# Performance work log

Hardware: AMD Instinct MI355X
Metric: run time of the kernel (lower is better)

## Reference

```python
import jax, jax.numpy as jnp
import numpy as np
from jax.scipy.linalg import solve_triangular

H, VD, M = 16, 64, 128
RIDGE = 0.01


def setup_inputs() -> dict:
    key = jax.random.key(0)
    ks = jax.random.split(key, 9)
    B, L, HD = 4, 2048, 1024
    s = 1.0 / np.sqrt(HD).astype(np.float32)
    return {
        "x": jax.random.normal(ks[0], (B, L, HD), dtype=jnp.float32),
        "cur_k": jnp.zeros((1,), dtype=jnp.float32),
        "input_mask": jnp.ones((B, L), dtype=jnp.float32),
        "Wq": jax.random.normal(ks[1], (HD, HD), dtype=jnp.float32) * s,
        "Wk": jax.random.normal(ks[2], (HD, HD), dtype=jnp.float32) * s,
        "Wv": jax.random.normal(ks[3], (HD, HD), dtype=jnp.float32) * s,
        "Wo": jax.random.normal(ks[4], (HD, HD), dtype=jnp.float32) * s,
        "bo": jax.random.normal(ks[5], (HD,), dtype=jnp.float32) * s,
        "rff_W": jax.random.normal(ks[6], (H, VD, M), dtype=jnp.float32),  # / lengthscale=1.0
        "rff_b": 2.0 * np.pi * jax.random.uniform(ks[7], (H, M), dtype=jnp.float32),
    }


def reference(x, cur_k, input_mask, Wq, Wk, Wv, Wo, bo, rff_W, rff_b):
    B, L, HD = x.shape
    scale = jnp.asarray(1.0 / np.sqrt(M), dtype=x.dtype)
    M2 = 2 * M

    def heads(t):  # [B,L,HD] -> [B,H,L,VD]
        return t.reshape(B, L, H, VD).transpose(0, 2, 1, 3)

    q = heads(x @ Wq.T)
    k = heads(x @ Wk.T)
    v = heads(x @ Wv.T)

    mask = input_mask[:, :L].astype(x.dtype)
    qmask = mask[:, None, :, None]  # [B,1,L,1]

    def rff(X):  # [B,H,L,VD] -> [B,H,L,2M]
        proj = jnp.einsum('bhld,hdm->bhlm', X, rff_W) + rff_b[None, :, None, :]
        return scale * jnp.concatenate([jnp.cos(proj), jnp.sin(proj)], axis=-1)

    PhiQ = rff(q)
    PhiK_w = rff(k) * qmask
    V_w = v * qmask

    G = jnp.einsum('bhlm,bhln->bhmn', PhiK_w, PhiK_w)  # [B,H,2M,2M]
    G = G + RIDGE * jnp.eye(M2, dtype=x.dtype)
    T = jnp.einsum('bhlm,bhld->bhmd', PhiK_w, V_w)      # [B,H,2M,VD]

    Lch = jnp.linalg.cholesky(G)
    y = solve_triangular(Lch, T, lower=True)
    W = solve_triangular(jnp.swapaxes(Lch, -2, -1), y, lower=False)

    out = jnp.einsum('bhlm,bhmd->bhld', PhiQ, W)        # [B,H,L,VD]
    # unsqueeze sample dim, permute to [B,1,L,H,VD], flatten heads -> [B,1,L,HD]
    samples = jnp.transpose(out, (0, 2, 1, 3)).reshape(B, L, HD)[:, None]
    samples = samples @ Wo.T + bo                        # W_O (dropout: eval no-op)
    samples = samples * qmask                            # [B,1,L,1] broadcast
    return samples
```

## Files before the change

kernel.cpp:

```cpp
#include <hip/hip_runtime.h>
#include <math.h>

#define B_ 4
#define L_ 2048
#define HD_ 1024
#define H_ 16
#define VD_ 64
#define M_ 128
#define M2_ 256
#define RIDGE_ 0.01f
#define SCALE_ 0.08838834764831845f

typedef unsigned short u16;
typedef __attribute__((ext_vector_type(8))) short short8;
typedef __attribute__((ext_vector_type(4))) float floatx4;

__device__ __forceinline__ u16 f2bf(float x) {
  unsigned u = __float_as_uint(x);
  unsigned r = u + 0x7fff + ((u >> 16) & 1);
  return (u16)(r >> 16);
}
__device__ __forceinline__ float bf2f(u16 h) {
  return __uint_as_float(((unsigned)h) << 16);
}
__device__ __forceinline__ void gload_lds16(const u16* g, u16* l) {
  __builtin_amdgcn_global_load_lds(
      (const __attribute__((address_space(1))) unsigned int*)g,
      (__attribute__((address_space(3))) unsigned int*)l, 16, 0, 0);
}
__device__ __forceinline__ void split4(float4 f, ushort4* h, float4* r) {
  h->x = f2bf(f.x); h->y = f2bf(f.y); h->z = f2bf(f.z); h->w = f2bf(f.w);
  r->x = f.x - bf2f(h->x); r->y = f.y - bf2f(h->y);
  r->z = f.z - bf2f(h->z); r->w = f.w - bf2f(h->w);
}

__global__ __launch_bounds__(256) void cvt_split_kernel(
    const float* __restrict__ src, u16* __restrict__ hi, u16* __restrict__ lo, int n4)
{
  int i = blockIdx.x * 256 + threadIdx.x;
  if (i < n4) {
    float4 f = ((const float4*)src)[i];
    ushort4 hv; float4 r;
    split4(f, &hv, &r);
    ushort4 lv = {f2bf(r.x), f2bf(r.y), f2bf(r.z), f2bf(r.w)};
    ((ushort4*)hi)[i] = hv;
    ((ushort4*)lo)[i] = lv;
  }
}

__global__ __launch_bounds__(256) void mfma_nt(
    const u16* __restrict__ A0, const u16* __restrict__ B0,
    float* __restrict__ C, int Ndim, int Kdim, int ldA, int ldB,
    const float* __restrict__ bias, const float* __restrict__ mask)
{
  __shared__ __align__(16) u16 a_sm[4096];
  __shared__ __align__(16) u16 b_sm[4096];
  const int tid = threadIdx.x;
  const int wave = tid >> 6, lane = tid & 63;
  const int m0 = blockIdx.y * 128, n0 = blockIdx.x * 128;
  const int wrow = (wave >> 1) * 64, wcol = (wave & 1) * 64;
  const int fm = lane & 15, q = lane >> 4;

  floatx4 acc[4][4];
#pragma unroll
  for (int i = 0; i < 4; ++i)
#pragma unroll
    for (int j = 0; j < 4; ++j) acc[i][j] = (floatx4){0.f, 0.f, 0.f, 0.f};

  const u16* Ag0 = A0 + (long)(m0 + lane) * ldA + wave * 8;
  const u16* Ag1 = A0 + (long)(m0 + 64 + lane) * ldA + wave * 8;
  const u16* Bg0 = B0 + (long)(n0 + lane) * ldB + wave * 8;
  const u16* Bg1 = B0 + (long)(n0 + 64 + lane) * ldB + wave * 8;
  u16* la0 = &a_sm[(wave * 128 + 0) * 8];
  u16* la1 = &a_sm[(wave * 128 + 64) * 8];
  u16* lb0 = &b_sm[(wave * 128 + 0) * 8];
  u16* lb1 = &b_sm[(wave * 128 + 64) * 8];

  for (int k0 = 0; k0 < Kdim; k0 += 32) {
    __syncthreads();
    gload_lds16(Ag0 + k0, la0);
    gload_lds16(Ag1 + k0, la1);
    gload_lds16(Bg0 + k0, lb0);
    gload_lds16(Bg1 + k0, lb1);
    __syncthreads();
    short8 af[4], bf[4];
#pragma unroll
    for (int i = 0; i < 4; ++i)
      af[i] = *(const short8*)&a_sm[(q * 128 + wrow + i * 16 + fm) * 8];
#pragma unroll
    for (int j = 0; j < 4; ++j)
      bf[j] = *(const short8*)&b_sm[(q * 128 + wcol + j * 16 + fm) * 8];
#pragma unroll
    for (int i = 0; i < 4; ++i)
#pragma unroll
      for (int j = 0; j < 4; ++j)
        acc[i][j] = __builtin_amdgcn_mfma_f32_16x16x32_bf16(af[i], bf[j], acc[i][j], 0, 0, 0);
  }

  const int colb = n0 + wcol + fm;
  const int rbase = m0 + wrow + (lane >> 4) * 4;
#pragma unroll
  for (int j = 0; j < 4; ++j) {
    int cg = colb + j * 16;
    float bb = bias ? bias[cg] : 0.f;
#pragma unroll
    for (int i = 0; i < 4; ++i) {
#pragma unroll
      for (int r = 0; r < 4; ++r) {
        int row = rbase + i * 16 + r;
        float val = acc[i][j][r];
        if (bias) val = (val + bb) * mask[row];
        C[(long)row * Ndim + cg] = val;
      }
    }
  }
}

__global__ __launch_bounds__(256) void mfma_nt3(
    const u16* __restrict__ Ah, const u16* __restrict__ Al,
    const u16* __restrict__ Bh, const u16* __restrict__ Bl,
    float* __restrict__ Cq, float* __restrict__ Ck, float* __restrict__ Cv)
{
  __shared__ __align__(16) u16 ah_sm[4096], al_sm[4096];
  __shared__ __align__(16) u16 bh_sm[4096], bl_sm[4096];
  const int tid = threadIdx.x;
  const int wave = tid >> 6, lane = tid & 63;
  const int m0 = blockIdx.y * 128, n0 = blockIdx.x * 128;
  const int wrow = (wave >> 1) * 64, wcol = (wave & 1) * 64;
  const int fm = lane & 15, q = lane >> 4;
  const bool vblk = (n0 >= 2048);

  floatx4 acc[4][4];
#pragma unroll
  for (int i = 0; i < 4; ++i)
#pragma unroll
    for (int j = 0; j < 4; ++j) acc[i][j] = (floatx4){0.f, 0.f, 0.f, 0.f};

  const long a0o = (long)(m0 + lane) * 1024 + wave * 8;
  const long a1o = (long)(m0 + 64 + lane) * 1024 + wave * 8;
  const long b0o = (long)(n0 + lane) * 1024 + wave * 8;
  const long b1o = (long)(n0 + 64 + lane) * 1024 + wave * 8;
  u16* lah0 = &ah_sm[(wave * 128 + 0) * 8];
  u16* lah1 = &ah_sm[(wave * 128 + 64) * 8];
  u16* lal0 = &al_sm[(wave * 128 + 0) * 8];
  u16* lal1 = &al_sm[(wave * 128 + 64) * 8];
  u16* lbh0 = &bh_sm[(wave * 128 + 0) * 8];
  u16* lbh1 = &bh_sm[(wave * 128 + 64) * 8];
  u16* lbl0 = &bl_sm[(wave * 128 + 0) * 8];
  u16* lbl1 = &bl_sm[(wave * 128 + 64) * 8];

  for (int k0 = 0; k0 < 1024; k0 += 32) {
    __syncthreads();
    gload_lds16(Ah + a0o + k0, lah0);
    gload_lds16(Ah + a1o + k0, lah1);
    gload_lds16(Bh + b0o + k0, lbh0);
    gload_lds16(Bh + b1o + k0, lbh1);
    if (!vblk) {
      gload_lds16(Al + a0o + k0, lal0);
      gload_lds16(Al + a1o + k0, lal1);
      gload_lds16(Bl + b0o + k0, lbl0);
      gload_lds16(Bl + b1o + k0, lbl1);
    }
    __syncthreads();
    short8 afh[4], bfh[4];
#pragma unroll
    for (int i = 0; i < 4; ++i)
      afh[i] = *(const short8*)&ah_sm[(q * 128 + wrow + i * 16 + fm) * 8];
#pragma unroll
    for (int j = 0; j < 4; ++j)
      bfh[j] = *(const short8*)&bh_sm[(q * 128 + wcol + j * 16 + fm) * 8];
    if (vblk) {
#pragma unroll
      for (int i = 0; i < 4; ++i)
#pragma unroll
        for (int j = 0; j < 4; ++j)
          acc[i][j] = __builtin_amdgcn_mfma_f32_16x16x32_bf16(afh[i], bfh[j], acc[i][j], 0, 0, 0);
    } else {
      short8 afl[4], bfl[4];
#pragma unroll
      for (int i = 0; i < 4; ++i)
        afl[i] = *(const short8*)&al_sm[(q * 128 + wrow + i * 16 + fm) * 8];
#pragma unroll
      for (int j = 0; j < 4; ++j)
        bfl[j] = *(const short8*)&bl_sm[(q * 128 + wcol + j * 16 + fm) * 8];
#pragma unroll
      for (int i = 0; i < 4; ++i)
#pragma unroll
        for (int j = 0; j < 4; ++j) {
          acc[i][j] = __builtin_amdgcn_mfma_f32_16x16x32_bf16(afh[i], bfh[j], acc[i][j], 0, 0, 0);
          acc[i][j] = __builtin_amdgcn_mfma_f32_16x16x32_bf16(afl[i], bfh[j], acc[i][j], 0, 0, 0);
          acc[i][j] = __builtin_amdgcn_mfma_f32_16x16x32_bf16(afh[i], bfl[j], acc[i][j], 0, 0, 0);
        }
    }
  }

  float* Cp; int cb;
  if (n0 < 1024)      { Cp = Cq; cb = n0; }
  else if (n0 < 2048) { Cp = Ck; cb = n0 - 1024; }
  else                { Cp = Cv; cb = n0 - 2048; }
  const int colb = cb + wcol + fm;
  const int rbase = m0 + wrow + (lane >> 4) * 4;
#pragma unroll
  for (int j = 0; j < 4; ++j) {
    int cg = colb + j * 16;
#pragma unroll
    for (int i = 0; i < 4; ++i)
#pragma unroll
      for (int r = 0; r < 4; ++r)
        Cp[(long)(rbase + i * 16 + r) * 1024 + cg] = acc[i][j][r];
  }
}

__global__ __launch_bounds__(256) void rff_k_t(
    const float* __restrict__ src, const float* __restrict__ mask,
    const float* __restrict__ rffW, const float* __restrict__ rffb,
    u16* __restrict__ pkh, u16* __restrict__ pkl, int b0)
{
  __shared__ __align__(16) float w_lds[64][132];
  __shared__ __align__(16) float x_lds[64][68];
  __shared__ float b_lds[128];
  const int l0 = blockIdx.x * 64;
  const int h = blockIdx.y, b = b0 + blockIdx.z;
  const int zloc = blockIdx.z * 16 + h;
  const int tid = threadIdx.x;

  const float* wsrc = rffW + h * 8192;
  for (int f = tid * 4; f < 8192; f += 1024) {
    int d = f >> 7, m = f & 127;
    *(float4*)&w_lds[d][m] = *(const float4*)&wsrc[f];
  }
  if (tid < 128) b_lds[tid] = rffb[h * 128 + tid];
  {
    int r = tid >> 2, c0 = (tid & 3) * 16;
    const float* srow = src + (long)(b * L_ + l0 + r) * 1024 + h * VD_ + c0;
    *(float4*)&x_lds[r][c0 + 0]  = *(const float4*)(srow + 0);
    *(float4*)&x_lds[r][c0 + 4]  = *(const float4*)(srow + 4);
    *(float4*)&x_lds[r][c0 + 8]  = *(const float4*)(srow + 8);
    *(float4*)&x_lds[r][c0 + 12] = *(const float4*)(srow + 12);
  }
  __syncthreads();

  const int ty = tid >> 4, tx = tid & 15;
  float acc[4][8];
  {
    float4 bb0 = *(const float4*)&b_lds[4 * tx];
    float4 bb1 = *(const float4*)&b_lds[4 * tx + 64];
#pragma unroll
    for (int i = 0; i < 4; ++i) {
      acc[i][0] = bb0.x; acc[i][1] = bb0.y; acc[i][2] = bb0.z; acc[i][3] = bb0.w;
      acc[i][4] = bb1.x; acc[i][5] = bb1.y; acc[i][6] = bb1.z; acc[i][7] = bb1.w;
    }
  }
#pragma unroll 8
  for (int kk = 0; kk < 64; ++kk) {
    float4 w0 = *(const float4*)&w_lds[kk][4 * tx];
    float4 w1 = *(const float4*)&w_lds[kk][4 * tx + 64];
    float xv[4];
#pragma unroll
    for (int i = 0; i < 4; ++i) xv[i] = x_lds[4 * ty + i][kk];
#pragma unroll
    for (int i = 0; i < 4; ++i) {
      acc[i][0] = fmaf(xv[i], w0.x, acc[i][0]);
      acc[i][1] = fmaf(xv[i], w0.y, acc[i][1]);
      acc[i][2] = fmaf(xv[i], w0.z, acc[i][2]);
      acc[i][3] = fmaf(xv[i], w0.w, acc[i][3]);
      acc[i][4] = fmaf(xv[i], w1.x, acc[i][4]);
      acc[i][5] = fmaf(xv[i], w1.y, acc[i][5]);
      acc[i][6] = fmaf(xv[i], w1.z, acc[i][6]);
      acc[i][7] = fmaf(xv[i], w1.w, acc[i][7]);
    }
  }
  float fi[4];
#pragma unroll
  for (int i = 0; i < 4; ++i) fi[i] = SCALE_ * mask[b * L_ + l0 + 4 * ty + i];
  float cvv[4][8], svv[4][8];
#pragma unroll
  for (int i = 0; i < 4; ++i)
#pragma unroll
    for (int jj = 0; jj < 8; ++jj) {
      float sv, cv;
      sincosf(acc[i][jj], &sv, &cv);
      cvv[i][jj] = cv * fi[i];
      svv[i][jj] = sv * fi[i];
    }
  const long lbase = l0 + 4 * ty;
  const long zbase = (long)zloc * 655360;
#pragma unroll
  for (int jj = 0; jj < 8; ++jj) {
    int mcol = (jj < 4) ? (4 * tx + jj) : (64 + 4 * tx + (jj - 4));
    ushort4 h4, l4;
    h4.x = f2bf(cvv[0][jj]); l4.x = f2bf(cvv[0][jj] - bf2f(h4.x));
    h4.y = f2bf(cvv[1][jj]); l4.y = f2bf(cvv[1][jj] - bf2f(h4.y));
    h4.z = f2bf(cvv[2][jj]); l4.z = f2bf(cvv[2][jj] - bf2f(h4.z));
    h4.w = f2bf(cvv[3][jj]); l4.w = f2bf(cvv[3][jj] - bf2f(h4.w));
    long base = zbase + (long)mcol * 2048 + lbase;
    *(ushort4*)&pkh[base] = h4;
    *(ushort4*)&pkl[base] = l4;
    ushort4 hs, ls;
    hs.x = f2bf(svv[0][jj]); ls.x = f2bf(svv[0][jj] - bf2f(hs.x));
    hs.y = f2bf(svv[1][jj]); ls.y = f2bf(svv[1][jj] - bf2f(hs.y));
    hs.z = f2bf(svv[2][jj]); ls.z = f2bf(svv[2][jj] - bf2f(hs.z));
    hs.w = f2bf(svv[3][jj]); ls.w = f2bf(svv[3][jj] - bf2f(hs.w));
    long base2 = zbase + (long)(mcol + 128) * 2048 + lbase;
    *(ushort4*)&pkh[base2] = hs;
    *(ushort4*)&pkl[base2] = ls;
  }
}

__global__ __launch_bounds__(256) void vt_kernel(
    const float* __restrict__ v, const float* __restrict__ mask,
    u16* __restrict__ pkh, u16* __restrict__ pkl, int b0)
{
  __shared__ float t[128][65];
  const int z = blockIdx.y;
  const int b = b0 + (z >> 4), h = z & 15;
  const int l0 = blockIdx.x * 128;
  const int tid = threadIdx.x;
  const int d = tid & 63, lg = tid >> 6;
  for (int i = 0; i < 128; i += 4) {
    int ll = i + lg;
    float mv = mask[b * L_ + l0 + ll];
    t[ll][d] = v[(long)(b * L_ + l0 + ll) * 1024 + h * 64 + d] * mv;
  }
  __syncthreads();
  const int d2 = tid >> 2, lofs = (tid & 3) * 32;
  long base = (long)z * 655360 + (long)(256 + d2) * 2048 + l0 + lofs;
  for (int j = 0; j < 32; j += 4) {
    float f0 = t[lofs + j + 0][d2], f1 = t[lofs + j + 1][d2];
    float f2 = t[lofs + j + 2][d2], f3 = t[lofs + j + 3][d2];
    ushort4 hv, lv;
    hv.x = f2bf(f0); lv.x = f2bf(f0 - bf2f(hv.x));
    hv.y = f2bf(f1); lv.y = f2bf(f1 - bf2f(hv.y));
    hv.z = f2bf(f2); lv.z = f2bf(f2 - bf2f(hv.z));
    hv.w = f2bf(f3); lv.w = f2bf(f3 - bf2f(hv.w));
    *(ushort4*)&pkh[base + j] = hv;
    *(ushort4*)&pkl[base + j] = lv;
  }
}

__global__ __launch_bounds__(256) void mfma_gt(
    const u16* __restrict__ pkh, const u16* __restrict__ pkl,
    float* __restrict__ G, float* __restrict__ T, int bh0)
{
  __shared__ __align__(16) u16 ah_sm[4096], al_sm[4096];
  __shared__ __align__(16) u16 bh_sm[2048], bl_sm[2048];
  const int tid = threadIdx.x;
  const int wave = tid >> 6, lane = tid & 63;
  const int z = blockIdx.z;
  const int m0 = blockIdx.y * 128, n0 = blockIdx.x * 64;
  const int wrow = (wave >> 1) * 64, wcol = (wave & 1) * 32;
  const int fm = lane & 15, q = lane >> 4;
  const long batch = (long)z * 655360;
  const u16* Ah = pkh + batch;
  const u16* Al = pkl + batch;

  floatx4 acc[4][2];
#pragma unroll
  for (int i = 0; i < 4; ++i)
#pragma unroll
    for (int j = 0; j < 2; ++j) acc[i][j] = (floatx4){0.f, 0.f, 0.f, 0.f};

  const long a0o = (long)(m0 + lane) * 2048 + wave * 8;
  const long a1o = (long)(m0 + 64 + lane) * 2048 + wave * 8;
  const long b0o = (long)(n0 + lane) * 2048 + wave * 8;
  u16* lah0 = &ah_sm[(wave * 128 + 0) * 8];
  u16* lah1 = &ah_sm[(wave * 128 + 64) * 8];
  u16* lal0 = &al_sm[(wave * 128 + 0) * 8];
  u16* lal1 = &al_sm[(wave * 128 + 64) * 8];
  u16* lbh = &bh_sm[(wave * 64) * 8];
  u16* lbl = &bl_sm[(wave * 64) * 8];

  for (int k0 = 0; k0 < 2048; k0 += 32) {
    __syncthreads();
    gload_lds16(Ah + a0o + k0, lah0);
    gload_lds16(Ah + a1o + k0, lah1);
    gload_lds16(Al + a0o + k0, lal0);
    gload_lds16(Al + a1o + k0, lal1);
    gload_lds16(Ah + b0o + k0, lbh);
    gload_lds16(Al + b0o + k0, lbl);
    __syncthreads();
    short8 afh[4], afl[4], bfh[2], bfl[2];
#pragma unroll
    for (int i = 0; i < 4; ++i) {
      afh[i] = *(const short8*)&ah_sm[(q * 128 + wrow + i * 16 + fm) * 8];
      afl[i] = *(const short8*)&al_sm[(q * 128 + wrow + i * 16 + fm) * 8];
    }
#pragma unroll
    for (int j = 0; j < 2; ++j) {
      bfh[j] = *(const short8*)&bh_sm[(q * 64 + wcol + j * 16 + fm) * 8];
      bfl[j] = *(const short8*)&bl_sm[(q * 64 + wcol + j * 16 + fm) * 8];
    }
#pragma unroll
    for (int i = 0; i < 4; ++i)
#pragma unroll
      for (int j = 0; j < 2; ++j) {
        acc[i][j] = __builtin_amdgcn_mfma_f32_16x16x32_bf16(afh[i], bfh[j], acc[i][j], 0, 0, 0);
        acc[i][j] = __builtin_amdgcn_mfma_f32_16x16x32_bf16(afl[i], bfh[j], acc[i][j], 0, 0, 0);
        acc[i][j] = __builtin_amdgcn_mfma_f32_16x16x32_bf16(afh[i], bfl[j], acc[i][j], 0, 0, 0);
      }
  }

  const int bh = bh0 + z;
  const int rbase = m0 + wrow + (lane >> 4) * 4;
#pragma unroll
  for (int j = 0; j < 2; ++j) {
    int col = n0 + wcol + j * 16 + fm;
#pragma unroll
    for (int i = 0; i < 4; ++i)
#pragma unroll
      for (int r = 0; r < 4; ++r) {
        int row = rbase + i * 16 + r;
        float val = acc[i][j][r];
        if (n0 < 256) G[(long)bh * 65536 + (long)row * 256 + col] = val;
        else T[(long)bh * 16384 + (long)row * 64 + (col - 256)] = val;
      }
  }
}

__global__ __launch_bounds__(256) void mfma_out_k(
    const u16* __restrict__ ph, const u16* __restrict__ pl,
    const u16* __restrict__ wth, const u16* __restrict__ wtl,
    u16* __restrict__ oh)
{
  __shared__ __align__(16) u16 ah_sm[4096], al_sm[4096];
  __shared__ __align__(16) u16 bh_sm[2048], bl_sm[2048];
  const int tid = threadIdx.x;
  const int wave = tid >> 6, lane = tid & 63;
  const int bh = blockIdx.y;
  const int b = bh >> 4, h = bh & 15;
  const int l0 = blockIdx.x * 128;
  const int wrow = (wave >> 1) * 64, wcol = (wave & 1) * 32;
  const int fm = lane & 15, q = lane >> 4;
  const u16* Ah = ph + (long)bh * 524288 + (long)l0 * 256;
  const u16* Al = pl + (long)bh * 524288 + (long)l0 * 256;
  const u16* Bh = wth + (long)bh * 16384;
  const u16* Bl = wtl + (long)bh * 16384;

  floatx4 acc[4][2];
#pragma unroll
  for (int i = 0; i < 4; ++i)
#pragma unroll
    for (int j = 0; j < 2; ++j) acc[i][j] = (floatx4){0.f, 0.f, 0.f, 0.f};

  const long a0o = (long)lane * 256 + wave * 8;
  const long a1o = (long)(64 + lane) * 256 + wave * 8;
  const long b0o = (long)lane * 256 + wave * 8;
  u16* lah0 = &ah_sm[(wave * 128 + 0) * 8];
  u16* lah1 = &ah_sm[(wave * 128 + 64) * 8];
  u16* lal0 = &al_sm[(wave * 128 + 0) * 8];
  u16* lal1 = &al_sm[(wave * 128 + 64) * 8];
  u16* lbh = &bh_sm[(wave * 64) * 8];
  u16* lbl = &bl_sm[(wave * 64) * 8];

  for (int k0 = 0; k0 < 256; k0 += 32) {
    __syncthreads();
    gload_lds16(Ah + a0o + k0, lah0);
    gload_lds16(Ah + a1o + k0, lah1);
    gload_lds16(Al + a0o + k0, lal0);
    gload_lds16(Al + a1o + k0, lal1);
    gload_lds16(Bh + b0o + k0, lbh);
    gload_lds16(Bl + b0o + k0, lbl);
    __syncthreads();
    short8 afh[4], afl[4], bfh[2], bfl[2];
#pragma unroll
    for (int i = 0; i < 4; ++i) {
      afh[i] = *(const short8*)&ah_sm[(q * 128 + wrow + i * 16 + fm) * 8];
      afl[i] = *(const short8*)&al_sm[(q * 128 + wrow + i * 16 + fm) * 8];
    }
#pragma unroll
    for (int j = 0; j < 2; ++j) {
      bfh[j] = *(const short8*)&bh_sm[(q * 64 + wcol + j * 16 + fm) * 8];
      bfl[j] = *(const short8*)&bl_sm[(q * 64 + wcol + j * 16 + fm) * 8];
    }
#pragma unroll
    for (int i = 0; i < 4; ++i)
#pragma unroll
      for (int j = 0; j < 2; ++j) {
        acc[i][j] = __builtin_amdgcn_mfma_f32_16x16x32_bf16(afh[i], bfh[j], acc[i][j], 0, 0, 0);
        acc[i][j] = __builtin_amdgcn_mfma_f32_16x16x32_bf16(afl[i], bfh[j], acc[i][j], 0, 0, 0);
        acc[i][j] = __builtin_amdgcn_mfma_f32_16x16x32_bf16(afh[i], bfl[j], acc[i][j], 0, 0, 0);
      }
  }

  const int rbase = l0 + wrow + (lane >> 4) * 4;
#pragma unroll
  for (int j = 0; j < 2; ++j) {
    int col = h * 64 + wcol + j * 16 + fm;
#pragma unroll
    for (int i = 0; i < 4; ++i)
#pragma unroll
      for (int r = 0; r < 4; ++r)
        oh[(long)(b * L_ + rbase + i * 16 + r) * 1024 + col] = f2bf(acc[i][j][r]);
  }
}

__global__ __launch_bounds__(512) void chol_rffq_wo_kernel(
    const float* __restrict__ G, float* __restrict__ Lg,
    const float* __restrict__ qsrc,
    const float* __restrict__ rffW, const float* __restrict__ rffb,
    u16* __restrict__ ph, u16* __restrict__ pl,
    const float* __restrict__ Wo, u16* __restrict__ wo_hi)
{
  extern __shared__ float sm[];
  const int bx = blockIdx.x;
  const int tid = threadIdx.x;

  if (bx < 64) {
    float* Lb = sm;
    const int bh = bx;
    const float* Gb = G + (long)bh * 65536;
    for (int f = tid; f < 136 * 256; f += 512) {
      int bi = f >> 8, e = f & 255;
      int i = e >> 4, j = e & 15;
      int I = 0; while ((I + 1) * (I + 2) / 2 <= bi) ++I;
      int J = bi - I * (I + 1) / 2;
      float v = Gb[(I * 16 + i) * 256 + J * 16 + j];
      if (I == J && i == j) v += RIDGE_;
      Lb[bi * 272 + i * 17 + j] = v;
    }
    __syncthreads();

    for (int p = 0; p < 16; ++p) {
      const int diagbase = (p * (p + 1) / 2 + p) * 272;
      if (tid < 64) {
        const int i = tid & 15;
        float r[16];
#pragma unroll
        for (int k = 0; k < 16; ++k) r[k] = Lb[diagbase + i * 17 + k];
#pragma unroll
        for (int j = 0; j < 16; ++j) {
          float dj = __shfl(r[j], j);
          float dinv = 1.0f / sqrtf(dj);
          r[j] *= dinv;
          float Lij = r[j];
#pragma unroll
          for (int k = j + 1; k < 16; ++k) {
            float Lkj = __shfl(r[j], k);
            r[k] = fmaf(-Lij, Lkj, r[k]);
          }
        }
        float x[16];
#pragma unroll
        for (int j = 0; j < 16; ++j) {
          float s = (i == j) ? 1.0f : 0.0f;
#pragma unroll
          for (int k = 0; k < j; ++k) {
            float Ljk = __shfl(r[k], j);
            s = fmaf(-Ljk, x[k], s);
          }
          float Ljj = __shfl(r[j], j);
          x[j] = s / Ljj;
        }
        if (tid < 16) {
#pragma unroll
          for (int j = 0; j < 16; ++j) Lb[diagbase + j * 17 + tid] = x[j];
        }
      }
      __syncthreads();

      const int nIb = 15 - p;
      const int tot = nIb * 256;
      float outv[8];
#pragma unroll
      for (int s = 0; s < 8; ++s) {
        int f = tid + s * 512;
        if (f < tot) {
          int Ib = f >> 8;
          int I = p + 1 + Ib;
          int e = f & 255;
          int i = e >> 4, j = e & 15;
          const float* Ablk = &Lb[(I * (I + 1) / 2 + p) * 272 + i * 17];
          const float* invD = &Lb[diagbase + j * 17];
          float s2 = 0.f;
#pragma unroll
          for (int k = 0; k < 16; ++k) s2 = fmaf(Ablk[k], invD[k], s2);
          outv[s] = s2;
        }
      }
      __syncthreads();
#pragma unroll
      for (int s = 0; s < 8; ++s) {
        int f = tid + s * 512;
        if (f < tot) {
          int Ib = f >> 8;
          int I = p + 1 + Ib;
          int e = f & 255;
          int i = e >> 4, j = e & 15;
          Lb[(I * (I + 1) / 2 + p) * 272 + i * 17 + j] = outv[s];
        }
      }
      __syncthreads();

      const int npairs = nIb * (nIb + 1) / 2;
      const int g = tid >> 4, t = tid & 15;
      const int tx = t & 3, ty = t >> 2;
      for (int pi0 = 0; pi0 < npairs; pi0 += 32) {
        int pi = pi0 + g;
        if (pi < npairs) {
          int a = 0; while ((a + 1) * (a + 2) / 2 <= pi) ++a;
          int b2 = pi - a * (a + 1) / 2;
          int I = p + 1 + a, J = p + 1 + b2;
          float* Cblk = &Lb[(I * (I + 1) / 2 + J) * 272];
          const float* Ablk = &Lb[(I * (I + 1) / 2 + p) * 272];
          const float* Bblk = &Lb[(J * (J + 1) / 2 + p) * 272];
          float c4[4][4];
#pragma unroll
          for (int ii = 0; ii < 4; ++ii)
#pragma unroll
            for (int jj = 0; jj < 4; ++jj)
              c4[ii][jj] = Cblk[(4 * ty + ii) * 17 + 4 * tx + jj];
#pragma unroll
          for (int kk = 0; kk < 16; ++kk) {
            float av[4], bv[4];
#pragma unroll
            for (int ii = 0; ii < 4; ++ii) av[ii] = Ablk[(4 * ty + ii) * 17 + kk];
#pragma unroll
            for (int jj = 0; jj < 4; ++jj) bv[jj] = Bblk[(4 * tx + jj) * 17 + kk];
#pragma unroll
            for (int ii = 0; ii < 4; ++ii)
#pragma unroll
              for (int jj = 0; jj < 4; ++jj)
                c4[ii][jj] = fmaf(-av[ii], bv[jj], c4[ii][jj]);
          }
#pragma unroll
          for (int ii = 0; ii < 4; ++ii)
#pragma unroll
            for (int jj = 0; jj < 4; ++jj)
              Cblk[(4 * ty + ii) * 17 + 4 * tx + jj] = c4[ii][jj];
        }
      }
      __syncthreads();
    }

    float* Lgb = Lg + (long)bh * 34816;
    for (int f = tid * 4; f < 136 * 256; f += 2048) {
      int bi = f >> 8, e = f & 255;
      int i = e >> 4, j = e & 15;
      float4 v;
      v.x = Lb[bi * 272 + i * 17 + j];
      v.y = Lb[bi * 272 + i * 17 + j + 1];
      v.z = Lb[bi * 272 + i * 17 + j + 2];
      v.w = Lb[bi * 272 + i * 17 + j + 3];
      *(float4*)&Lgb[f] = v;
    }
  } else if (bx < 64 + 1024) {
    const int id = bx - 64;
    const int l0 = (id & 15) * 128;
    const int h = (id >> 4) & 15;
    const int b = id >> 8;
    float* w_lds = sm;
    float* x_lds = sm + 8448;
    float* b_lds = sm + 8448 + 8704;

    const float* wsrc = rffW + h * 8192;
    for (int f = tid * 4; f < 8192; f += 2048) {
      int d = f >> 7, m = f & 127;
      *(float4*)&w_lds[d * 132 + m] = *(const float4*)&wsrc[f];
    }
    if (tid < 128) b_lds[tid] = rffb[h * 128 + tid];
    {
      int r = tid >> 2, c0 = (tid & 3) * 16;
      const float* srow = qsrc + (long)(b * L_ + l0 + r) * 1024 + h * VD_ + c0;
      *(float4*)&x_lds[r * 68 + c0 + 0]  = *(const float4*)(srow + 0);
      *(float4*)&x_lds[r * 68 + c0 + 4]  = *(const float4*)(srow + 4);
      *(float4*)&x_lds[r * 68 + c0 + 8]  = *(const float4*)(srow + 8);
      *(float4*)&x_lds[r * 68 + c0 + 12] = *(const float4*)(srow + 12);
    }
    __syncthreads();

    const int sub = tid >> 8;
    const int t = tid & 255;
    const int ty = t >> 4, tx = t & 15;
    const int rrow = sub * 64 + 4 * ty;
    float acc[4][8];
    {
      float4 bb0 = *(const float4*)&b_lds[4 * tx];
      float4 bb1 = *(const float4*)&b_lds[4 * tx + 64];
#pragma unroll
      for (int i = 0; i < 4; ++i) {
        acc[i][0] = bb0.x; acc[i][1] = bb0.y; acc[i][2] = bb0.z; acc[i][3] = bb0.w;
        acc[i][4] = bb1.x; acc[i][5] = bb1.y; acc[i][6] = bb1.z; acc[i][7] = bb1.w;
      }
    }
#pragma unroll 8
    for (int kk = 0; kk < 64; ++kk) {
      float4 w0 = *(const float4*)&w_lds[kk * 132 + 4 * tx];
      float4 w1 = *(const float4*)&w_lds[kk * 132 + 4 * tx + 64];
      float xv[4];
#pragma unroll
      for (int i = 0; i < 4; ++i) xv[i] = x_lds[(rrow + i) * 68 + kk];
#pragma unroll
      for (int i = 0; i < 4; ++i) {
        acc[i][0] = fmaf(xv[i], w0.x, acc[i][0]);
        acc[i][1] = fmaf(xv[i], w0.y, acc[i][1]);
        acc[i][2] = fmaf(xv[i], w0.z, acc[i][2]);
        acc[i][3] = fmaf(xv[i], w0.w, acc[i][3]);
        acc[i][4] = fmaf(xv[i], w1.x, acc[i][4]);
        acc[i][5] = fmaf(xv[i], w1.y, acc[i][5]);
        acc[i][6] = fmaf(xv[i], w1.z, acc[i][6]);
        acc[i][7] = fmaf(xv[i], w1.w, acc[i][7]);
      }
    }
#pragma unroll
    for (int i = 0; i < 4; ++i) {
      int l = l0 + rrow + i;
      float4 c0, c1, s0, s1;
      float sv, cv;
      sincosf(acc[i][0], &sv, &cv); c0.x = cv * SCALE_; s0.x = sv * SCALE_;
      sincosf(acc[i][1], &sv, &cv); c0.y = cv * SCALE_; s0.y = sv * SCALE_;
      sincosf(acc[i][2], &sv, &cv); c0.z = cv * SCALE_; s0.z = sv * SCALE_;
      sincosf(acc[i][3], &sv, &cv); c0.w = cv * SCALE_; s0.w = sv * SCALE_;
      sincosf(acc[i][4], &sv, &cv); c1.x = cv * SCALE_; s1.x = sv * SCALE_;
      sincosf(acc[i][5], &sv, &cv); c1.y = cv * SCALE_; s1.y = sv * SCALE_;
      sincosf(acc[i][6], &sv, &cv); c1.z = cv * SCALE_; s1.z = sv * SCALE_;
      sincosf(acc[i][7], &sv, &cv); c1.w = cv * SCALE_; s1.w = sv * SCALE_;
      long base = ((long)(b * H_ + h) * L_ + l) * M2_;
      ushort4 hv; float4 r4;
      split4(c0, &hv, &r4);
      *(ushort4*)&ph[base + 4 * tx] = hv;
      *(ushort4*)&pl[base + 4 * tx] = (ushort4){f2bf(r4.x), f2bf(r4.y), f2bf(r4.z), f2bf(r4.w)};
      split4(c1, &hv, &r4);
      *(ushort4*)&ph[base + 64 + 4 * tx] = hv;
      *(ushort4*)&pl[base + 64 + 4 * tx] = (ushort4){f2bf(r4.x), f2bf(r4.y), f2bf(r4.z), f2bf(r4.w)};
      split4(s0, &hv, &r4);
      *(ushort4*)&ph[base + 128 + 4 * tx] = hv;
      *(ushort4*)&pl[base + 128 + 4 * tx] = (ushort4){f2bf(r4.x), f2bf(r4.y), f2bf(r4.z), f2bf(r4.w)};
      split4(s1, &hv, &r4);
      *(ushort4*)&ph[base + 192 + 4 * tx] = hv;
      *(ushort4*)&pl[base + 192 + 4 * tx] = (ushort4){f2bf(r4.x), f2bf(r4.y), f2bf(r4.z), f2bf(r4.w)};
    }
  } else {
    const int id2 = bx - (64 + 1024);
    int idx = id2 * 512 + tid;
    for (int i = idx; i < 262144; i += 65536) {
      float4 f = ((const float4*)Wo)[i];
      ushort4 hv = {f2bf(f.x), f2bf(f.y), f2bf(f.z), f2bf(f.w)};
      ((ushort4*)wo_hi)[i] = hv;
    }
  }
}

__global__ __launch_bounds__(256) void tri_solve_kernel(
    const float* __restrict__ Lg, const float* __restrict__ T,
    float* __restrict__ Wt)
{
  __shared__ float Y[256 * 17];
  __shared__ float tmp[16 * 17];
  const int bh = blockIdx.y;
  const int d0 = blockIdx.x * 16;
  const int tid = threadIdx.x;
  const int i = tid >> 4, d = tid & 15;
  const float* Lb = Lg + (long)bh * 34816;
  const float* Tb = T + (long)bh * 16384;

  for (int r = i; r < 256; r += 16) Y[r * 17 + d] = Tb[r * 64 + d0 + d];
  __syncthreads();

  for (int J = 0; J < 16; ++J) {
    float acc = Y[(J * 16 + i) * 17 + d];
    for (int c = 0; c < J; ++c) {
      const float* Lblk = &Lb[(J * (J + 1) / 2 + c) * 256 + i * 16];
#pragma unroll
      for (int k = 0; k < 16; k += 4) {
        float4 l4 = *(const float4*)&Lblk[k];
        acc = fmaf(-l4.x, Y[(c * 16 + k + 0) * 17 + d], acc);
        acc = fmaf(-l4.y, Y[(c * 16 + k + 1) * 17 + d], acc);
        acc = fmaf(-l4.z, Y[(c * 16 + k + 2) * 17 + d], acc);
        acc = fmaf(-l4.w, Y[(c * 16 + k + 3) * 17 + d], acc);
      }
    }
    tmp[i * 17 + d] = acc;
    __syncthreads();
    const float* invD = &Lb[(J * (J + 1) / 2 + J) * 256 + i * 16];
    float y = 0.f;
#pragma unroll
    for (int k = 0; k < 16; ++k) y = fmaf(invD[k], tmp[k * 17 + d], y);
    Y[(J * 16 + i) * 17 + d] = y;
    __syncthreads();
  }

  for (int J = 15; J >= 0; --J) {
    float acc = Y[(J * 16 + i) * 17 + d];
    for (int I = J + 1; I < 16; ++I) {
      const float* Lblk = &Lb[(I * (I + 1) / 2 + J) * 256];
#pragma unroll
      for (int k = 0; k < 16; ++k)
        acc = fmaf(-Lblk[k * 16 + i], Y[(I * 16 + k) * 17 + d], acc);
    }
    tmp[i * 17 + d] = acc;
    __syncthreads();
    const float* invD = &Lb[(J * (J + 1) / 2 + J) * 256];
    float w = 0.f;
#pragma unroll
    for (int k = 0; k < 16; ++k) w = fmaf(invD[k * 16 + i], tmp[k * 17 + d], w);
    Y[(J * 16 + i) * 17 + d] = w;
    __syncthreads();
  }

  for (int f = tid; f < 16 * 256; f += 256) {
    int dc = f >> 8, m = f & 255;
    Wt[(long)bh * 16384 + (long)(d0 + dc) * 256 + m] = Y[m * 17 + dc];
  }
}

__global__ void ws_too_small_kernel(float* out) { out[0] = 12345.0f; }

extern "C" void kernel_launch(void* const* d_in, const int* in_sizes, int n_in,
                              void* d_out, int out_size, void* d_ws, size_t ws_size,
                              hipStream_t stream) {
  const float* x    = (const float*)d_in[0];
  const float* mask = (const float*)d_in[2];
  const float* Wq   = (const float*)d_in[3];
  const float* Wk   = (const float*)d_in[4];
  const float* Wv   = (const float*)d_in[5];
  const float* Wo   = (const float*)d_in[6];
  const float* bo   = (const float*)d_in[7];
  const float* rffW = (const float*)d_in[8];
  const float* rffb = (const float*)d_in[9];
  float* out = (float*)d_out;
  float* ws  = (float*)d_ws;

  const size_t needed = 58720256UL * 4UL;
  if (ws_size < needed) {
    ws_too_small_kernel<<<1, 1, 0, stream>>>(out);
    return;
  }
  float* q = ws;
  u16* oh_bf = (u16*)ws;
  float* kbuf = ws + 8388608;
  float* T    = ws + 8388608;
  float* G    = ws + 9437184;
  float* Lg   = ws + 13631488;
  u16* big16 = (u16*)(ws + 16777216);
  u16* x_hi = big16;
  u16* x_lo = big16 + 8388608;
  u16* w_hi = big16 + 16777216;
  u16* w_lo = big16 + 19922944;
  u16* pk_hi = big16;
  u16* pk_lo = big16 + 20971520;
  u16* phiq_hi = big16;
  u16* phiq_lo = big16 + 33554432;
  float* v = ws + 50331648;
  float* wt_f = ws + 50331648;
  u16* wt_hi = (u16*)(ws + 51380224);
  u16* wt_lo = wt_hi + 1048576;
  u16* wo_hi = wt_hi + 2097152;

  hipFuncSetAttribute((const void*)chol_rffq_wo_kernel,
                      hipFuncAttributeMaxDynamicSharedMemorySize, 147968);

  dim3 blk(256);

  cvt_split_kernel<<<8192, blk, 0, stream>>>(x, x_hi, x_lo, 2097152);
  cvt_split_kernel<<<1024, blk, 0, stream>>>(Wq, w_hi,           w_lo,           262144);
  cvt_split_kernel<<<1024, blk, 0, stream>>>(Wk, w_hi + 1048576, w_lo + 1048576, 262144);
  cvt_split_kernel<<<1024, blk, 0, stream>>>(Wv, w_hi + 2097152, w_lo + 2097152, 262144);

  mfma_nt3<<<dim3(24, 64), blk, 0, stream>>>(x_hi, x_lo, w_hi, w_lo, q, kbuf, v);

  for (int half = 0; half < 2; ++half) {
    int b0 = half * 2, bh0 = half * 32;
    rff_k_t<<<dim3(32, 16, 2), blk, 0, stream>>>(kbuf, mask, rffW, rffb, pk_hi, pk_lo, b0);
    vt_kernel<<<dim3(16, 32), blk, 0, stream>>>(v, mask, pk_hi, pk_lo, b0);
    mfma_gt<<<dim3(5, 2, 32), blk, 0, stream>>>(pk_hi, pk_lo, G, T, bh0);
  }

  chol_rffq_wo_kernel<<<dim3(64 + 1024 + 128), dim3(512), 147968, stream>>>(
      G, Lg, q, rffW, rffb, phiq_hi, phiq_lo, Wo, wo_hi);

  tri_solve_kernel<<<dim3(4, 64), dim3(256), 0, stream>>>(Lg, T, wt_f);
  cvt_split_kernel<<<1024, blk, 0, stream>>>(wt_f, wt_hi, wt_lo, 262144);

  mfma_out_k<<<dim3(16, 64), blk, 0, stream>>>(phiq_hi, phiq_lo, wt_hi, wt_lo, oh_bf);

  mfma_nt<<<dim3(8, 64), blk, 0, stream>>>(oh_bf, wo_hi, out, 1024, 1024, 1024, 1024, bo, mask);
}
```

Before: 969.5 us.

## Split-K the G/T Gram GEMM, separate V projection, fuse Wt bf16 split

The G/T Gram GEMM now splits the 2048-long reduction into two halves across twice as many blocks. Partial results go to separate buffers and a new reduction kernel sums them, giving more parallelism from the small 5x2x32 grid. The fused QKV projection is split into a Q/K-only kernel that always uses the 3-term hi/lo product, plus a plain single-term mfma_nt for V. This removes the per-block branch. The triangular solve now writes bf16 hi/lo directly, dropping a separate conversion kernel launch and its fp32 round-trip, at the cost of extra partial-buffer traffic and one more launch.

```diff
diff --git a/kernel.cpp b/kernel.cpp
--- a/kernel.cpp
+++ b/kernel.cpp
@@ -116,10 +116,10 @@
   }
 }
 
-__global__ __launch_bounds__(256) void mfma_nt3(
+__global__ __launch_bounds__(256) void mfma_qk3(
     const u16* __restrict__ Ah, const u16* __restrict__ Al,
     const u16* __restrict__ Bh, const u16* __restrict__ Bl,
-    float* __restrict__ Cq, float* __restrict__ Ck, float* __restrict__ Cv)
+    float* __restrict__ Cq, float* __restrict__ Ck)
 {
   __shared__ __align__(16) u16 ah_sm[4096], al_sm[4096];
   __shared__ __align__(16) u16 bh_sm[4096], bl_sm[4096];
@@ -128,7 +128,6 @@
   const int m0 = blockIdx.y * 128, n0 = blockIdx.x * 128;
   const int wrow = (wave >> 1) * 64, wcol = (wave & 1) * 64;
   const int fm = lane & 15, q = lane >> 4;
-  const bool vblk = (n0 >= 2048);
 
   floatx4 acc[4][4];
 #pragma unroll
@@ -153,51 +152,37 @@
     __syncthreads();
     gload_lds16(Ah + a0o + k0, lah0);
     gload_lds16(Ah + a1o + k0, lah1);
+    gload_lds16(Al + a0o + k0, lal0);
+    gload_lds16(Al + a1o + k0, lal1);
     gload_lds16(Bh + b0o + k0, lbh0);
     gload_lds16(Bh + b1o + k0, lbh1);
-    if (!vblk) {
-      gload_lds16(Al + a0o + k0, lal0);
-      gload_lds16(Al + a1o + k0, lal1);
-      gload_lds16(Bl + b0o + k0, lbl0);
-      gload_lds16(Bl + b1o + k0, lbl1);
-    }
-    __syncthreads();
-    short8 afh[4], bfh[4];
+    gload_lds16(Bl + b0o + k0, lbl0);
+    gload_lds16(Bl + b1o + k0, lbl1);
+    __syncthreads();
+    short8 afh[4], afl[4], bfh[4], bfl[4];
+#pragma unroll
+    for (int i = 0; i < 4; ++i) {
+      afh[i] = *(const short8*)&ah_sm[(q * 128 + wrow + i * 16 + fm) * 8];
+      afl[i] = *(const short8*)&al_sm[(q * 128 + wrow + i * 16 + fm) * 8];
+    }
+#pragma unroll
+    for (int j = 0; j < 4; ++j) {
+      bfh[j] = *(const short8*)&bh_sm[(q * 128 + wcol + j * 16 + fm) * 8];
+      bfl[j] = *(const short8*)&bl_sm[(q * 128 + wcol + j * 16 + fm) * 8];
+    }
 #pragma unroll
     for (int i = 0; i < 4; ++i)
-      afh[i] = *(const short8*)&ah_sm[(q * 128 + wrow + i * 16 + fm) * 8];
-#pragma unroll
-    for (int j = 0; j < 4; ++j)
-      bfh[j] = *(const short8*)&bh_sm[(q * 128 + wcol + j * 16 + fm) * 8];
-    if (vblk) {
-#pragma unroll
-      for (int i = 0; i < 4; ++i)
-#pragma unroll
-        for (int j = 0; j < 4; ++j)
-          acc[i][j] = __builtin_amdgcn_mfma_f32_16x16x32_bf16(afh[i], bfh[j], acc[i][j], 0, 0, 0);
-    } else {
-      short8 afl[4], bfl[4];
-#pragma unroll
-      for (int i = 0; i < 4; ++i)
-        afl[i] = *(const short8*)&al_sm[(q * 128 + wrow + i * 16 + fm) * 8];
-#pragma unroll
-      for (int j = 0; j < 4; ++j)
-        bfl[j] = *(const short8*)&bl_sm[(q * 128 + wcol + j * 16 + fm) * 8];
-#pragma unroll
-      for (int i = 0; i < 4; ++i)
-#pragma unroll
-        for (int j = 0; j < 4; ++j) {
-          acc[i][j] = __builtin_amdgcn_mfma_f32_16x16x32_bf16(afh[i], bfh[j], acc[i][j], 0, 0, 0);
-          acc[i][j] = __builtin_amdgcn_mfma_f32_16x16x32_bf16(afl[i], bfh[j], acc[i][j], 0, 0, 0);
-          acc[i][j] = __builtin_amdgcn_mfma_f32_16x16x32_bf16(afh[i], bfl[j], acc[i][j], 0, 0, 0);
-        }
-    }
+#pragma unroll
+      for (int j = 0; j < 4; ++j) {
+        acc[i][j] = __builtin_amdgcn_mfma_f32_16x16x32_bf16(afh[i], bfh[j], acc[i][j], 0, 0, 0);
+        acc[i][j] = __builtin_amdgcn_mfma_f32_16x16x32_bf16(afl[i], bfh[j], acc[i][j], 0, 0, 0);
+        acc[i][j] = __builtin_amdgcn_mfma_f32_16x16x32_bf16(afh[i], bfl[j], acc[i][j], 0, 0, 0);
+      }
   }
 
   float* Cp; int cb;
-  if (n0 < 1024)      { Cp = Cq; cb = n0; }
-  else if (n0 < 2048) { Cp = Ck; cb = n0 - 1024; }
-  else                { Cp = Cv; cb = n0 - 2048; }
+  if (n0 < 1024) { Cp = Cq; cb = n0; }
+  else           { Cp = Ck; cb = n0 - 1024; }
   const int colb = cb + wcol + fm;
   const int rbase = m0 + wrow + (lane >> 4) * 4;
 #pragma unroll
@@ -340,14 +325,15 @@
 
 __global__ __launch_bounds__(256) void mfma_gt(
     const u16* __restrict__ pkh, const u16* __restrict__ pkl,
-    float* __restrict__ G, float* __restrict__ T, int bh0)
+    float* __restrict__ Gp, float* __restrict__ Tp, int bh0)
 {
   __shared__ __align__(16) u16 ah_sm[4096], al_sm[4096];
   __shared__ __align__(16) u16 bh_sm[2048], bl_sm[2048];
   const int tid = threadIdx.x;
   const int wave = tid >> 6, lane = tid & 63;
   const int z = blockIdx.z;
-  const int m0 = blockIdx.y * 128, n0 = blockIdx.x * 64;
+  const int mt = blockIdx.y & 1, kc = blockIdx.y >> 1;
+  const int m0 = mt * 128, n0 = blockIdx.x * 64;
   const int wrow = (wave >> 1) * 64, wcol = (wave & 1) * 32;
   const int fm = lane & 15, q = lane >> 4;
   const long batch = (long)z * 655360;
@@ -370,7 +356,8 @@
   u16* lbh = &bh_sm[(wave * 64) * 8];
   u16* lbl = &bl_sm[(wave * 64) * 8];
 
-  for (int k0 = 0; k0 < 2048; k0 += 32) {
+  const int kbeg = kc * 1024, kend = kbeg + 1024;
+  for (int k0 = kbeg; k0 < kend; k0 += 32) {
     __syncthreads();
     gload_lds16(Ah + a0o + k0, lah0);
     gload_lds16(Ah + a1o + k0, lah1);
@@ -401,6 +388,8 @@
   }
 
   const int bh = bh0 + z;
+  float* Gb = Gp + (long)kc * 4194304;
+  float* Tb = Tp + (long)kc * 1048576;
   const int rbase = m0 + wrow + (lane >> 4) * 4;
 #pragma unroll
   for (int j = 0; j < 2; ++j) {
@@ -411,9 +400,28 @@
       for (int r = 0; r < 4; ++r) {
         int row = rbase + i * 16 + r;
         float val = acc[i][j][r];
-        if (n0 < 256) G[(long)bh * 65536 + (long)row * 256 + col] = val;
-        else T[(long)bh * 16384 + (long)row * 64 + (col - 256)] = val;
-      }
+        if (n0 < 256) Gb[(long)bh * 65536 + (long)row * 256 + col] = val;
+        else Tb[(long)bh * 16384 + (long)row * 64 + (col - 256)] = val;
+      }
+  }
+}
+
+__global__ __launch_bounds__(256) void reduce_gt_kernel(
+    const float* __restrict__ Gp, float* __restrict__ G,
+    const float* __restrict__ Tp, float* __restrict__ T)
+{
+  long i = (long)blockIdx.x * 256 + threadIdx.x;
+  if (i < 1048576) {
+    float4 a = ((const float4*)Gp)[i];
+    float4 b = ((const float4*)(Gp + 4194304))[i];
+    float4 o = {a.x + b.x, a.y + b.y, a.z + b.z, a.w + b.w};
+    ((float4*)G)[i] = o;
+  } else {
+    long j = i - 1048576;
+    float4 a = ((const float4*)Tp)[j];
+    float4 b = ((const float4*)(Tp + 1048576))[j];
+    float4 o = {a.x + b.x, a.y + b.y, a.z + b.z, a.w + b.w};
+    ((float4*)T)[j] = o;
   }
 }
 
@@ -742,7 +750,7 @@
 
 __global__ __launch_bounds__(256) void tri_solve_kernel(
     const float* __restrict__ Lg, const float* __restrict__ T,
-    float* __restrict__ Wt)
+    u16* __restrict__ wth, u16* __restrict__ wtl)
 {
   __shared__ float Y[256 * 17];
   __shared__ float tmp[16 * 17];
@@ -799,7 +807,11 @@
 
   for (int f = tid; f < 16 * 256; f += 256) {
     int dc = f >> 8, m = f & 255;
-    Wt[(long)bh * 16384 + (long)(d0 + dc) * 256 + m] = Y[m * 17 + dc];
+    float val = Y[m * 17 + dc];
+    u16 h = f2bf(val);
+    long o = (long)bh * 16384 + (long)(d0 + dc) * 256 + m;
+    wth[o] = h;
+    wtl[o] = f2bf(val - bf2f(h));
   }
 }
 
@@ -838,11 +850,12 @@
   u16* w_lo = big16 + 19922944;
   u16* pk_hi = big16;
   u16* pk_lo = big16 + 20971520;
+  float* Gp = ws + 37748736;
+  float* Tp = ws + 46137344;
   u16* phiq_hi = big16;
   u16* phiq_lo = big16 + 33554432;
   float* v = ws + 50331648;
-  float* wt_f = ws + 50331648;
-  u16* wt_hi = (u16*)(ws + 51380224);
+  u16* wt_hi = (u16*)(ws + 50331648);
   u16* wt_lo = wt_hi + 1048576;
   u16* wo_hi = wt_hi + 2097152;
 
@@ -856,20 +869,23 @@
   cvt_split_kernel<<<1024, blk, 0, stream>>>(Wk, w_hi + 1048576, w_lo + 1048576, 262144);
   cvt_split_kernel<<<1024, blk, 0, stream>>>(Wv, w_hi + 2097152, w_lo + 2097152, 262144);
 
-  mfma_nt3<<<dim3(24, 64), blk, 0, stream>>>(x_hi, x_lo, w_hi, w_lo, q, kbuf, v);
+  mfma_qk3<<<dim3(16, 64), blk, 0, stream>>>(x_hi, x_lo, w_hi, w_lo, q, kbuf);
+  mfma_nt<<<dim3(8, 64), blk, 0, stream>>>(x_hi, w_hi + 2097152, v,
+                                           1024, 1024, 1024, 1024, nullptr, nullptr);
 
   for (int half = 0; half < 2; ++half) {
     int b0 = half * 2, bh0 = half * 32;
     rff_k_t<<<dim3(32, 16, 2), blk, 0, stream>>>(kbuf, mask, rffW, rffb, pk_hi, pk_lo, b0);
     vt_kernel<<<dim3(16, 32), blk, 0, stream>>>(v, mask, pk_hi, pk_lo, b0);
-    mfma_gt<<<dim3(5, 2, 32), blk, 0, stream>>>(pk_hi, pk_lo, G, T, bh0);
-  }
+    mfma_gt<<<dim3(5, 4, 32), blk, 0, stream>>>(pk_hi, pk_lo, Gp, Tp, bh0);
+  }
+
+  reduce_gt_kernel<<<5120, blk, 0, stream>>>(Gp, G, Tp, T);
 
   chol_rffq_wo_kernel<<<dim3(64 + 1024 + 128), dim3(512), 147968, stream>>>(
       G, Lg, q, rffW, rffb, phiq_hi, phiq_lo, Wo, wo_hi);
 
-  tri_solve_kernel<<<dim3(4, 64), dim3(256), 0, stream>>>(Lg, T, wt_f);
-  cvt_split_kernel<<<1024, blk, 0, stream>>>(wt_f, wt_hi, wt_lo, 262144);
+  tri_solve_kernel<<<dim3(4, 64), dim3(256), 0, stream>>>(Lg, T, wt_hi, wt_lo);
 
   mfma_out_k<<<dim3(16, 64), blk, 0, stream>>>(phiq_hi, phiq_lo, wt_hi, wt_lo, oh_bf);
 
```

Measured after the change: 958.6 us. About the same (-1.1%).
